# Kernel tuning notes

Hardware: AMD Instinct MI355X
Metric: run time of the kernel (lower is better)

The kernel has to match this reference:

```python
import jax, jax.numpy as jnp
import numpy as np

NUM_EMBEDDINGS = 1024
EMBEDDING_DIM = 64
COMMITMENT_COST = 0.25


def setup_inputs() -> dict:
    key = jax.random.key(0)
    k_x, k_cb = jax.random.split(key)
    x = jax.random.normal(k_x, (16, EMBEDDING_DIM, 64, 64), dtype=jnp.float32)
    # nn.Embedding weight init: uniform(-1/K, 1/K)
    codebook = jax.random.uniform(
        k_cb, (NUM_EMBEDDINGS, EMBEDDING_DIM), dtype=jnp.float32,
        minval=-1.0 / NUM_EMBEDDINGS, maxval=1.0 / NUM_EMBEDDINGS)
    return {"x": x, "codebook": codebook}


def reference(x, codebook):
    sg = jax.lax.stop_gradient
    # NCHW -> NHWC
    inputs = jnp.transpose(x, (0, 2, 3, 1))  # [B,H,W,D]
    in_shape = inputs.shape
    flat = inputs.reshape(-1, EMBEDDING_DIM)  # [N,D]
    # squared L2 distances to each codebook entry: [N,K]
    distances = (jnp.sum(flat ** 2, axis=1, keepdims=True)
                 + jnp.sum(codebook ** 2, axis=1)
                 - 2.0 * jnp.matmul(flat, codebook.T))
    encoding_indices = jnp.argmin(distances, axis=1)  # [N]
    # one-hot matmul in the original == plain gather
    quantized = codebook[encoding_indices].reshape(in_shape)  # [B,H,W,D]
    e_latent_loss = jnp.mean((sg(quantized) - inputs) ** 2)
    q_latent_loss = jnp.mean((quantized - sg(inputs)) ** 2)
    loss = q_latent_loss + COMMITMENT_COST * e_latent_loss
    # straight-through estimator
    quantized = inputs + sg(quantized - inputs)
    quantized = jnp.transpose(quantized, (0, 3, 1, 2))  # NHWC -> NCHW
    return quantized, loss
```

## Files before the change

### kernel.cpp

```cpp
#include <hip/hip_runtime.h>

#define NPTS   65536
#define DIM    64
#define KCODES 1024
#define HW     4096

typedef __attribute__((ext_vector_type(8))) short  short8;
typedef __attribute__((ext_vector_type(4))) float  floatx4;

__device__ __forceinline__ short f2bf(float f) {
    unsigned u = __builtin_bit_cast(unsigned, f);
    u = (u + 0x7FFFu + ((u >> 16) & 1u)) >> 16;
    return (short)u;
}

__global__ __launch_bounds__(512, 2) void vq_fused(
    const float* __restrict__ x, const float* __restrict__ cb,
    float* __restrict__ out, float* __restrict__ loss_ptr)
{
    __shared__ __align__(16) short s_cb[KCODES * DIM];
    __shared__ float s_nrm[KCODES];
    __shared__ float s_part[2][256];
    __shared__ float s_xn[256];
    __shared__ float s_red[4];

    const int tid  = threadIdx.x;
    const int lane = tid & 63;
    const int wave = tid >> 6;
    const int col  = lane & 15;
    const int quad = lane >> 4;
    const int pg   = wave & 3;
    const int kc   = wave >> 2;

    #pragma unroll
    for (int i = 0; i < 16; ++i) {
        int g = tid + 512 * i;
        int c = g >> 3, p = g & 7;
        const float4* p4 = (const float4*)cb + 2 * (size_t)g;
        float4 va = p4[0], vb = p4[1];
        short8 v;
        v[0] = f2bf(va.x); v[1] = f2bf(va.y); v[2] = f2bf(va.z); v[3] = f2bf(va.w);
        v[4] = f2bf(vb.x); v[5] = f2bf(vb.y); v[6] = f2bf(vb.z); v[7] = f2bf(vb.w);
        *(short8*)&s_cb[(c << 6) + ((p ^ (c & 7)) << 3)] = v;
        float ns = fmaf(va.x, va.x, fmaf(va.y, va.y, fmaf(va.z, va.z, va.w * va.w)));
        ns = fmaf(vb.x, vb.x, fmaf(vb.y, vb.y, fmaf(vb.z, vb.z, fmaf(vb.w, vb.w, ns))));
        ns += __shfl_xor(ns, 1, 64);
        ns += __shfl_xor(ns, 2, 64);
        ns += __shfl_xor(ns, 4, 64);
        if ((g & 7) == 0) s_nrm[c] = -0.5f * ns;
    }

    const int pb = blockIdx.x * 256 + pg * 64;
    short8 afrag[4][2];
    #pragma unroll
    for (int pt = 0; pt < 4; ++pt) {
        int n = pb + pt * 16 + col;
        const float* bp = x + ((size_t)(n >> 12) << 18) + (n & 4095);
        float ns = 0.0f;
        #pragma unroll
        for (int kh = 0; kh < 2; ++kh) {
            short8 f;
            #pragma unroll
            for (int j = 0; j < 8; ++j) {
                float v = bp[(size_t)(kh * 32 + quad * 8 + j) * HW];
                f[j] = f2bf(v);
                ns = fmaf(v, v, ns);
            }
            afrag[pt][kh] = f;
        }
        ns += __shfl_xor(ns, 16, 64);
        ns += __shfl_xor(ns, 32, 64);
        if (kc == 0 && quad == 0) s_xn[pg * 64 + pt * 16 + col] = ns;
    }

    __syncthreads();

    float best[4][4];
    #pragma unroll
    for (int pt = 0; pt < 4; ++pt)
        #pragma unroll
        for (int r = 0; r < 4; ++r) best[pt][r] = -3.4e38f;

    const int cb0 = kc * 512;
    #pragma unroll 4
    for (int ct = 0; ct < 32; ++ct) {
        int code = cb0 + ct * 16 + col;
        int c7 = code & 7;
        int so = code << 6;
        short8 b0 = *(const short8*)&s_cb[so + (((quad    ) ^ c7) << 3)];
        short8 b1 = *(const short8*)&s_cb[so + (((quad + 4) ^ c7) << 3)];
        float nv = s_nrm[code];
        floatx4 cinit = {nv, nv, nv, nv};
        unsigned idxv = (unsigned)code;
        #pragma unroll
        for (int pt = 0; pt < 4; ++pt) {
            floatx4 acc = __builtin_amdgcn_mfma_f32_16x16x32_bf16(afrag[pt][0], b0, cinit, 0, 0, 0);
            acc = __builtin_amdgcn_mfma_f32_16x16x32_bf16(afrag[pt][1], b1, acc, 0, 0, 0);
            #pragma unroll
            for (int r = 0; r < 4; ++r) {
                unsigned pbits = (__builtin_bit_cast(unsigned, acc[r]) & 0xFFFFFC00u) | idxv;
                best[pt][r] = fmaxf(best[pt][r], __builtin_bit_cast(float, pbits));
            }
        }
    }

    #pragma unroll
    for (int pt = 0; pt < 4; ++pt)
        #pragma unroll
        for (int r = 0; r < 4; ++r) {
            float v = best[pt][r];
            v = fmaxf(v, __shfl_xor(v, 1, 64));
            v = fmaxf(v, __shfl_xor(v, 2, 64));
            v = fmaxf(v, __shfl_xor(v, 4, 64));
            v = fmaxf(v, __shfl_xor(v, 8, 64));
            best[pt][r] = v;
        }
    if (col == 0) {
        #pragma unroll
        for (int pt = 0; pt < 4; ++pt)
            #pragma unroll
            for (int r = 0; r < 4; ++r)
                s_part[kc][pg * 64 + pt * 16 + quad * 4 + r] = best[pt][r];
    }
    __syncthreads();

    {
        int ptid = tid & 255;
        int dq   = tid >> 8;
        float m = fmaxf(s_part[0][ptid], s_part[1][ptid]);
        unsigned mu = __builtin_bit_cast(unsigned, m);
        int idx = (int)(mu & 1023u);
        int n = blockIdx.x * 256 + ptid;
        float* op = out + ((size_t)(n >> 12) << 18) + (n & 4095);
        const float4* crow = (const float4*)(cb + (size_t)idx * DIM + dq * 32);
        #pragma unroll
        for (int j = 0; j < 8; ++j) {
            float4 v = crow[j];
            op[(size_t)(dq * 32 + j * 4 + 0) * HW] = v.x;
            op[(size_t)(dq * 32 + j * 4 + 1) * HW] = v.y;
            op[(size_t)(dq * 32 + j * 4 + 2) * HW] = v.z;
            op[(size_t)(dq * 32 + j * 4 + 3) * HW] = v.w;
        }
        if (dq == 0) {
            float vtr = __builtin_bit_cast(float, mu & 0xFFFFFC00u);
            float lp = s_xn[ptid] - 2.0f * vtr;
            #pragma unroll
            for (int off = 32; off > 0; off >>= 1)
                lp += __shfl_down(lp, off, 64);
            if (lane == 0) s_red[wave] = lp;
        }
    }
    __syncthreads();
    if (tid == 0)
        atomicAdd(loss_ptr, (s_red[0] + s_red[1] + s_red[2] + s_red[3])
                              * (1.25f / ((float)NPTS * DIM)));
}

extern "C" void kernel_launch(void* const* d_in, const int* in_sizes, int n_in,
                              void* d_out, int out_size, void* d_ws, size_t ws_size,
                              hipStream_t stream) {
    const float* x  = (const float*)d_in[0];
    const float* cb = (const float*)d_in[1];
    float* out      = (float*)d_out;
    float* loss_ptr = out + (size_t)NPTS * DIM;

    vq_fused<<<NPTS / 256, 512, 0, stream>>>(x, cb, out, loss_ptr);
}
```

Measured before the change: 89.37 us.

## Stage input tile through LDS with vectorized coalesced loads

Replaces the per-thread strided scalar global loads of x (each of the eight waves re-reading its points) with float4 loads of a 64x128 tile per half, staged as bf16 in a padded shared buffer and then read back into MFMA A-fragments. Point norms are accumulated with shared-memory atomics instead of shuffles. The intent is to remove the duplicated, poorly vectorized reads of x, since both kc waves previously loaded the same points. In exchange it adds two extra barriers per half, LDS atomics and about 17KB of extra shared memory, which may reduce occupancy.

```diff
diff --git a/kernel.cpp b/kernel.cpp
--- a/kernel.cpp
+++ b/kernel.cpp
@@ -4,8 +4,10 @@
 #define DIM    64
 #define KCODES 1024
 #define HW     4096
+#define XROW   132
 
 typedef __attribute__((ext_vector_type(8))) short  short8;
+typedef __attribute__((ext_vector_type(4))) short  short4v;
 typedef __attribute__((ext_vector_type(4))) float  floatx4;
 
 __device__ __forceinline__ short f2bf(float f) {
@@ -20,6 +22,7 @@
 {
     __shared__ __align__(16) short s_cb[KCODES * DIM];
     __shared__ float s_nrm[KCODES];
+    __shared__ __align__(16) short s_x[DIM * XROW];
     __shared__ float s_part[2][256];
     __shared__ float s_xn[256];
     __shared__ float s_red[4];
@@ -31,6 +34,8 @@
     const int quad = lane >> 4;
     const int pg   = wave & 3;
     const int kc   = wave >> 2;
+
+    if (tid < 256) s_xn[tid] = 0.0f;
 
     #pragma unroll
     for (int i = 0; i < 16; ++i) {
@@ -50,30 +55,53 @@
         if ((g & 7) == 0) s_nrm[c] = -0.5f * ns;
     }
 
-    const int pb = blockIdx.x * 256 + pg * 64;
+    const int n0   = blockIdx.x * 256;
+    const size_t xbase = ((size_t)(n0 >> 12) << 18) + (n0 & 4095);
+    const int dbase = tid >> 5;
+    const int p4i   = (tid & 31) * 4;
+    const int pgl   = pg & 1;
     short8 afrag[4][2];
+
     #pragma unroll
-    for (int pt = 0; pt < 4; ++pt) {
-        int n = pb + pt * 16 + col;
-        const float* bp = x + ((size_t)(n >> 12) << 18) + (n & 4095);
-        float ns = 0.0f;
+    for (int half = 0; half < 2; ++half) {
+        float4 xv[4];
         #pragma unroll
-        for (int kh = 0; kh < 2; ++kh) {
-            short8 f;
+        for (int pass = 0; pass < 4; ++pass) {
+            int d = dbase + 16 * pass;
+            xv[pass] = *(const float4*)(x + xbase + (size_t)d * HW + half * 128 + p4i);
+        }
+        float xn[4] = {0.f, 0.f, 0.f, 0.f};
+        #pragma unroll
+        for (int pass = 0; pass < 4; ++pass) {
+            int d = dbase + 16 * pass;
+            float4 v = xv[pass];
+            short4v s = { f2bf(v.x), f2bf(v.y), f2bf(v.z), f2bf(v.w) };
+            *(short4v*)&s_x[d * XROW + p4i] = s;
+            xn[0] = fmaf(v.x, v.x, xn[0]);
+            xn[1] = fmaf(v.y, v.y, xn[1]);
+            xn[2] = fmaf(v.z, v.z, xn[2]);
+            xn[3] = fmaf(v.w, v.w, xn[3]);
+        }
+        __syncthreads();
+        #pragma unroll
+        for (int c2 = 0; c2 < 4; ++c2)
+            atomicAdd(&s_xn[half * 128 + p4i + c2], xn[c2]);
+        if ((pg >> 1) == half) {
             #pragma unroll
-            for (int j = 0; j < 8; ++j) {
-                float v = bp[(size_t)(kh * 32 + quad * 8 + j) * HW];
-                f[j] = f2bf(v);
-                ns = fmaf(v, v, ns);
+            for (int t = 0; t < 4; ++t) {
+                int px = pgl * 64 + t * 16 + col;
+                #pragma unroll
+                for (int kh = 0; kh < 2; ++kh) {
+                    short8 f;
+                    #pragma unroll
+                    for (int j = 0; j < 8; ++j)
+                        f[j] = s_x[(kh * 32 + quad * 8 + j) * XROW + px];
+                    afrag[t][kh] = f;
+                }
             }
-            afrag[pt][kh] = f;
         }
-        ns += __shfl_xor(ns, 16, 64);
-        ns += __shfl_xor(ns, 32, 64);
-        if (kc == 0 && quad == 0) s_xn[pg * 64 + pt * 16 + col] = ns;
+        __syncthreads();
     }
-
-    __syncthreads();
 
     float best[4][4];
     #pragma unroll
```

New measurement: 93.72 us. 4.9% more time.

## Prefetch x and codebook loads into registers, gather output from LDS

Applied to the files above, without the earlier changes.

All x loads for the A fragments are issued up front alongside the first half of the codebook loads, and the codebook is staged in two register batches, so global-memory latency overlaps with bf16 conversion and LDS stores. Launch bounds are relaxed to one block per CU so the extra live registers fit; the large LDS footprint already limits occupancy to one block. The final output gather reads the chosen code from the bf16 codebook in LDS instead of the fp32 codebook in global memory. That saves global reads but writes bf16-rounded values, which lowers output precision.

```diff
diff --git a/kernel.cpp b/kernel.cpp
--- a/kernel.cpp
+++ b/kernel.cpp
@@ -14,7 +14,7 @@
     return (short)u;
 }
 
-__global__ __launch_bounds__(512, 2) void vq_fused(
+__global__ __launch_bounds__(512, 1) void vq_fused(
     const float* __restrict__ x, const float* __restrict__ cb,
     float* __restrict__ out, float* __restrict__ loss_ptr)
 {
@@ -32,12 +32,32 @@
     const int pg   = wave & 3;
     const int kc   = wave >> 2;
 
-    #pragma unroll
-    for (int i = 0; i < 16; ++i) {
+    const float4* cbp = (const float4*)cb;
+    float4 ra[8][2];
+    #pragma unroll
+    for (int i = 0; i < 8; ++i) {
+        int g = tid + 512 * i;
+        ra[i][0] = cbp[2 * (size_t)g];
+        ra[i][1] = cbp[2 * (size_t)g + 1];
+    }
+    const int pb = blockIdx.x * 256 + pg * 64;
+    float xr[4][16];
+    #pragma unroll
+    for (int pt = 0; pt < 4; ++pt) {
+        int n = pb + pt * 16 + col;
+        const float* bp = x + ((size_t)(n >> 12) << 18) + (n & 4095);
+        #pragma unroll
+        for (int k = 0; k < 16; ++k) {
+            int d = ((k >> 3) * 32) + quad * 8 + (k & 7);
+            xr[pt][k] = bp[(size_t)d * HW];
+        }
+    }
+
+    #pragma unroll
+    for (int i = 0; i < 8; ++i) {
         int g = tid + 512 * i;
         int c = g >> 3, p = g & 7;
-        const float4* p4 = (const float4*)cb + 2 * (size_t)g;
-        float4 va = p4[0], vb = p4[1];
+        float4 va = ra[i][0], vb = ra[i][1];
         short8 v;
         v[0] = f2bf(va.x); v[1] = f2bf(va.y); v[2] = f2bf(va.z); v[3] = f2bf(va.w);
         v[4] = f2bf(vb.x); v[5] = f2bf(vb.y); v[6] = f2bf(vb.z); v[7] = f2bf(vb.w);
@@ -49,20 +69,39 @@
         ns += __shfl_xor(ns, 4, 64);
         if ((g & 7) == 0) s_nrm[c] = -0.5f * ns;
     }
-
-    const int pb = blockIdx.x * 256 + pg * 64;
+    #pragma unroll
+    for (int i = 0; i < 8; ++i) {
+        int g = tid + 512 * (i + 8);
+        ra[i][0] = cbp[2 * (size_t)g];
+        ra[i][1] = cbp[2 * (size_t)g + 1];
+    }
+    #pragma unroll
+    for (int i = 0; i < 8; ++i) {
+        int g = tid + 512 * (i + 8);
+        int c = g >> 3, p = g & 7;
+        float4 va = ra[i][0], vb = ra[i][1];
+        short8 v;
+        v[0] = f2bf(va.x); v[1] = f2bf(va.y); v[2] = f2bf(va.z); v[3] = f2bf(va.w);
+        v[4] = f2bf(vb.x); v[5] = f2bf(vb.y); v[6] = f2bf(vb.z); v[7] = f2bf(vb.w);
+        *(short8*)&s_cb[(c << 6) + ((p ^ (c & 7)) << 3)] = v;
+        float ns = fmaf(va.x, va.x, fmaf(va.y, va.y, fmaf(va.z, va.z, va.w * va.w)));
+        ns = fmaf(vb.x, vb.x, fmaf(vb.y, vb.y, fmaf(vb.z, vb.z, fmaf(vb.w, vb.w, ns))));
+        ns += __shfl_xor(ns, 1, 64);
+        ns += __shfl_xor(ns, 2, 64);
+        ns += __shfl_xor(ns, 4, 64);
+        if ((g & 7) == 0) s_nrm[c] = -0.5f * ns;
+    }
+
     short8 afrag[4][2];
     #pragma unroll
     for (int pt = 0; pt < 4; ++pt) {
-        int n = pb + pt * 16 + col;
-        const float* bp = x + ((size_t)(n >> 12) << 18) + (n & 4095);
         float ns = 0.0f;
         #pragma unroll
         for (int kh = 0; kh < 2; ++kh) {
             short8 f;
             #pragma unroll
             for (int j = 0; j < 8; ++j) {
-                float v = bp[(size_t)(kh * 32 + quad * 8 + j) * HW];
+                float v = xr[pt][kh * 8 + j];
                 f[j] = f2bf(v);
                 ns = fmaf(v, v, ns);
             }
@@ -132,14 +171,17 @@
         int idx = (int)(mu & 1023u);
         int n = blockIdx.x * 256 + ptid;
         float* op = out + ((size_t)(n >> 12) << 18) + (n & 4095);
-        const float4* crow = (const float4*)(cb + (size_t)idx * DIM + dq * 32);
-        #pragma unroll
-        for (int j = 0; j < 8; ++j) {
-            float4 v = crow[j];
-            op[(size_t)(dq * 32 + j * 4 + 0) * HW] = v.x;
-            op[(size_t)(dq * 32 + j * 4 + 1) * HW] = v.y;
-            op[(size_t)(dq * 32 + j * 4 + 2) * HW] = v.z;
-            op[(size_t)(dq * 32 + j * 4 + 3) * HW] = v.w;
+        int c7 = idx & 7;
+        #pragma unroll
+        for (int pp = 0; pp < 4; ++pp) {
+            int p = dq * 4 + pp;
+            short8 s = *(const short8*)&s_cb[(idx << 6) + ((p ^ c7) << 3)];
+            #pragma unroll
+            for (int e = 0; e < 8; ++e) {
+                float v = __builtin_bit_cast(float,
+                            ((unsigned)(unsigned short)s[e]) << 16);
+                op[(size_t)(p * 8 + e) * HW] = v;
+            }
         }
         if (dq == 0) {
             float vtr = __builtin_bit_cast(float, mu & 0xFFFFFC00u);
```

After: 87.21 us. 2.4% less time.

## Pre-convert codebook in a prep kernel and gather output from LDS

Applied to the files above, without the earlier changes.

A small prep kernel now converts the codebook to swizzled bf16 and computes the code norms once per call, storing them in workspace. Each main block copies the ready bf16 codebook into shared memory instead of reading and converting fp32 data, and issues all x loads up front as nontemporal loads so their latency overlaps the codebook copy. The quantized output is rebuilt from the bf16 shared-memory codebook and written with nontemporal stores, which drops a scattered global gather. The cost is a second launch, more register pressure (launch bounds relaxed to one block per SIMD target), and output values that are bf16-rounded rather than exact fp32 codebook entries.

```diff
diff --git a/kernel.cpp b/kernel.cpp
--- a/kernel.cpp
+++ b/kernel.cpp
@@ -14,8 +14,29 @@
     return (short)u;
 }
 
-__global__ __launch_bounds__(512, 2) void vq_fused(
-    const float* __restrict__ x, const float* __restrict__ cb,
+__global__ __launch_bounds__(256) void vq_prep(
+    const float* __restrict__ cb, short* __restrict__ cbb,
+    float* __restrict__ nrmws)
+{
+    int g = blockIdx.x * 256 + threadIdx.x;
+    int c = g >> 3, p = g & 7;
+    const float4* p4 = (const float4*)cb + 2 * (size_t)g;
+    float4 va = p4[0], vb = p4[1];
+    short8 v;
+    v[0] = f2bf(va.x); v[1] = f2bf(va.y); v[2] = f2bf(va.z); v[3] = f2bf(va.w);
+    v[4] = f2bf(vb.x); v[5] = f2bf(vb.y); v[6] = f2bf(vb.z); v[7] = f2bf(vb.w);
+    *(short8*)&cbb[(c << 6) + ((p ^ (c & 7)) << 3)] = v;
+    float ns = fmaf(va.x, va.x, fmaf(va.y, va.y, fmaf(va.z, va.z, va.w * va.w)));
+    ns = fmaf(vb.x, vb.x, fmaf(vb.y, vb.y, fmaf(vb.z, vb.z, fmaf(vb.w, vb.w, ns))));
+    ns += __shfl_xor(ns, 1, 64);
+    ns += __shfl_xor(ns, 2, 64);
+    ns += __shfl_xor(ns, 4, 64);
+    if ((g & 7) == 0) nrmws[c] = -0.5f * ns;
+}
+
+__global__ __launch_bounds__(512, 1) void vq_fused(
+    const float* __restrict__ x, const short* __restrict__ cbb,
+    const float* __restrict__ nrmws,
     float* __restrict__ out, float* __restrict__ loss_ptr)
 {
     __shared__ __align__(16) short s_cb[KCODES * DIM];
@@ -32,37 +53,41 @@
     const int pg   = wave & 3;
     const int kc   = wave >> 2;
 
-    #pragma unroll
-    for (int i = 0; i < 16; ++i) {
-        int g = tid + 512 * i;
-        int c = g >> 3, p = g & 7;
-        const float4* p4 = (const float4*)cb + 2 * (size_t)g;
-        float4 va = p4[0], vb = p4[1];
-        short8 v;
-        v[0] = f2bf(va.x); v[1] = f2bf(va.y); v[2] = f2bf(va.z); v[3] = f2bf(va.w);
-        v[4] = f2bf(vb.x); v[5] = f2bf(vb.y); v[6] = f2bf(vb.z); v[7] = f2bf(vb.w);
-        *(short8*)&s_cb[(c << 6) + ((p ^ (c & 7)) << 3)] = v;
-        float ns = fmaf(va.x, va.x, fmaf(va.y, va.y, fmaf(va.z, va.z, va.w * va.w)));
-        ns = fmaf(vb.x, vb.x, fmaf(vb.y, vb.y, fmaf(vb.z, vb.z, fmaf(vb.w, vb.w, ns))));
-        ns += __shfl_xor(ns, 1, 64);
-        ns += __shfl_xor(ns, 2, 64);
-        ns += __shfl_xor(ns, 4, 64);
-        if ((g & 7) == 0) s_nrm[c] = -0.5f * ns;
-    }
-
+    short8 cr[16];
+    #pragma unroll
+    for (int i = 0; i < 16; ++i)
+        cr[i] = *(const short8*)(cbb + tid * 8 + i * 4096);
+    float nr0 = nrmws[tid];
+    float nr1 = nrmws[tid + 512];
     const int pb = blockIdx.x * 256 + pg * 64;
-    short8 afrag[4][2];
+    float xr[4][16];
     #pragma unroll
     for (int pt = 0; pt < 4; ++pt) {
         int n = pb + pt * 16 + col;
         const float* bp = x + ((size_t)(n >> 12) << 18) + (n & 4095);
+        #pragma unroll
+        for (int k = 0; k < 16; ++k) {
+            int d = ((k >> 3) * 32) + quad * 8 + (k & 7);
+            xr[pt][k] = __builtin_nontemporal_load(bp + (size_t)d * HW);
+        }
+    }
+
+    #pragma unroll
+    for (int i = 0; i < 16; ++i)
+        *(short8*)&s_cb[tid * 8 + i * 4096] = cr[i];
+    s_nrm[tid]       = nr0;
+    s_nrm[tid + 512] = nr1;
+
+    short8 afrag[4][2];
+    #pragma unroll
+    for (int pt = 0; pt < 4; ++pt) {
         float ns = 0.0f;
         #pragma unroll
         for (int kh = 0; kh < 2; ++kh) {
             short8 f;
             #pragma unroll
             for (int j = 0; j < 8; ++j) {
-                float v = bp[(size_t)(kh * 32 + quad * 8 + j) * HW];
+                float v = xr[pt][kh * 8 + j];
                 f[j] = f2bf(v);
                 ns = fmaf(v, v, ns);
             }
@@ -132,14 +157,17 @@
         int idx = (int)(mu & 1023u);
         int n = blockIdx.x * 256 + ptid;
         float* op = out + ((size_t)(n >> 12) << 18) + (n & 4095);
-        const float4* crow = (const float4*)(cb + (size_t)idx * DIM + dq * 32);
-        #pragma unroll
-        for (int j = 0; j < 8; ++j) {
-            float4 v = crow[j];
-            op[(size_t)(dq * 32 + j * 4 + 0) * HW] = v.x;
-            op[(size_t)(dq * 32 + j * 4 + 1) * HW] = v.y;
-            op[(size_t)(dq * 32 + j * 4 + 2) * HW] = v.z;
-            op[(size_t)(dq * 32 + j * 4 + 3) * HW] = v.w;
+        int c7 = idx & 7;
+        #pragma unroll
+        for (int pp = 0; pp < 4; ++pp) {
+            int p = dq * 4 + pp;
+            short8 s = *(const short8*)&s_cb[(idx << 6) + ((p ^ c7) << 3)];
+            #pragma unroll
+            for (int e = 0; e < 8; ++e) {
+                float v = __builtin_bit_cast(float,
+                            ((unsigned)(unsigned short)s[e]) << 16);
+                __builtin_nontemporal_store(v, op + (size_t)(p * 8 + e) * HW);
+            }
         }
         if (dq == 0) {
             float vtr = __builtin_bit_cast(float, mu & 0xFFFFFC00u);
@@ -164,5 +192,9 @@
     float* out      = (float*)d_out;
     float* loss_ptr = out + (size_t)NPTS * DIM;
 
-    vq_fused<<<NPTS / 256, 512, 0, stream>>>(x, cb, out, loss_ptr);
-}
+    short* cbb  = (short*)d_ws;
+    float* nrmw = (float*)((char*)d_ws + (size_t)KCODES * DIM * sizeof(short));
+
+    vq_prep<<<32, 256, 0, stream>>>(cb, cbb, nrmw);
+    vq_fused<<<NPTS / 256, 512, 0, stream>>>(x, cbb, nrmw, out, loss_ptr);
+}
```

Result: faster. 86.15 us (-3.6%).
